# Optimization experiments

Hardware: AMD Instinct MI355X
Metric: run time of the kernel (lower is better)

The kernel has to match this reference:

```python
import jax, jax.numpy as jnp
import numpy as np

SEQ, BS, IN, H, NUM_LAYERS = 512, 64, 1024, 1024, 2


def setup_inputs() -> dict:
    key = jax.random.key(0)
    k1, k2, k3, k4 = jax.random.split(key, 4)

    def xavier(k, shape):
        fan_in, fan_out = shape
        lim = jnp.sqrt(6.0 / (fan_in + fan_out))
        return jax.random.uniform(k, shape, jnp.float32, -lim, lim)

    return {
        "x": jax.random.normal(k1, (SEQ, BS, IN), jnp.float32),
        "W_ii0": xavier(k2, (IN, 4 * H)),
        "W_ii": xavier(k3, (H, 4 * H)),
        "W_hi": xavier(k4, (H, 4 * H)),
        "bias": jnp.zeros((4 * H,), jnp.float32),
    }


def _run_layer(x, W_in, W_hi, bias, hidden):
    # x: [seq, bs, feat]; precompute input projection for all timesteps at once
    xw = jnp.einsum('sbf,fg->sbg', x, W_in) + bias  # [seq, bs, 4H]
    bs = x.shape[1]

    def step(carry, xw_t):
        h, c = carry
        gates = xw_t + h @ W_hi  # [bs, 4H]
        i_t = jax.nn.sigmoid(gates[:, :hidden])
        f_t = jax.nn.sigmoid(gates[:, hidden:2 * hidden])
        g_t = jnp.tanh(gates[:, 2 * hidden:3 * hidden])
        o_t = jax.nn.sigmoid(gates[:, 3 * hidden:])
        c = f_t * c + i_t * g_t
        h = o_t * jnp.tanh(c)
        return (h, c), h

    h0 = jnp.zeros((bs, hidden), x.dtype)
    c0 = jnp.zeros((bs, hidden), x.dtype)
    (h, c), hs = jax.lax.scan(step, (h0, c0), xw)
    return hs, h, c  # hs: [seq, bs, hidden]


def reference(x, W_ii0, W_ii, W_hi, bias):
    h = c = None
    for l in range(NUM_LAYERS):
        W_in = W_ii0 if l == 0 else W_ii
        x, h, c = _run_layer(x, W_in, W_hi, bias, H)
    return x, (h, c)
```

## Files before the change

kernel.cpp:

```cpp
#include <hip/hip_runtime.h>

typedef __attribute__((ext_vector_type(8))) short short8;
typedef __attribute__((ext_vector_type(4))) short short4v;
typedef __attribute__((ext_vector_type(4))) float floatx4;

#define SEQ 512
#define BS  64
#define HID 1024
#define G4  4096
#define NBLK 128
#define NGRP 4
#define BPG  32
#define GBS  16
#define UPB  32

__device__ __forceinline__ unsigned short f2b(float f) {
  union { float f; unsigned u; } v; v.f = f;
  return (unsigned short)((v.u + 0x7FFFu + ((v.u >> 16) & 1u)) >> 16);
}
__device__ __forceinline__ float b2f(unsigned short s) {
  union { unsigned u; float f; } v; v.u = ((unsigned)s) << 16;
  return v.f;
}

__device__ __forceinline__ void gload_lds16_cc(const void* g, void* l) {
  __builtin_amdgcn_global_load_lds(
      (const __attribute__((address_space(1))) unsigned int*)g,
      (__attribute__((address_space(3))) unsigned int*)l,
      16, 0, 17);
}

__global__ void wtrans(const float* __restrict__ W, short* __restrict__ WT) {
  __shared__ float tile[32][33];
  const int tx = threadIdx.x, ty = threadIdx.y;
  const int n0 = blockIdx.x << 5, k0 = blockIdx.y << 5;
#pragma unroll
  for (int i = 0; i < 32; i += 8)
    tile[ty + i][tx] = W[(size_t)(k0 + ty + i) * G4 + n0 + tx];
  __syncthreads();
#pragma unroll
  for (int i = 0; i < 32; i += 8)
    WT[(size_t)(n0 + ty + i) * 1024 + k0 + tx] = (short)f2b(tile[tx][ty + i]);
}

__global__ __launch_bounds__(256)
void conv_bf16(const float* __restrict__ in, unsigned short* __restrict__ out) {
  const size_t i = ((size_t)blockIdx.x * 256 + threadIdx.x) * 8;
  const floatx4 a = *(const floatx4*)(in + i);
  const floatx4 b = *(const floatx4*)(in + i + 4);
  short8 s;
#pragma unroll
  for (int e = 0; e < 4; ++e) { s[e] = (short)f2b(a[e]); s[4 + e] = (short)f2b(b[e]); }
  *(short8*)(out + i) = s;
}

struct FusedArgs {
  const unsigned short* xw;
  const short* wt_hi;
  unsigned short* hbuf;
  float* cbuf;
  unsigned int* flags;
  float* hs;
  unsigned short* hsb;
  float* h_final;
  float* c_final;
  int t0, t1, wr_final;
  const short* A;
  const short* BT;
  const float* bias;
  unsigned short* dst;
  int Mrows, genable;
};

__device__ __forceinline__ void scan_body(const FusedArgs& p, char* smem) {
  float* gsm = (float*)(smem + 32768);
  const int tid = threadIdx.x;
  const int wave = tid >> 6, lane = tid & 63;
  const int lr = lane & 15, lh = lane >> 4;
  const int nt = wave >> 1;
  const int kh = wave & 1;
  const int blk = blockIdx.x;
  const int g = blk >> 5;
  const int ub_idx = blk & 31;
  const int gcol = ((nt >> 1) << 10) + ub_idx * UPB + ((nt & 1) << 4) + lr;

  short8 breg[16];
  {
    const short* wp = p.wt_hi + (size_t)gcol * HID + (kh << 9) + (lh << 3);
#pragma unroll
    for (int kk = 0; kk < 16; ++kk) breg[kk] = *(const short8*)(wp + (kk << 5));
  }

  const int b_loc = tid >> 5, u_loc = tid & 31;
  const int ci = ((g * GBS + b_loc) << 10) + ub_idx * UPB + u_loc;
  float creg = (tid < 512) ? p.cbuf[ci] : 0.f;

  const int asw = lr & 7;
  const unsigned long long fad =
      (unsigned long long)(p.flags + ((size_t)(g * BPG) + (lane & 31)) * 16);

  for (int t = p.t0; t < p.t1; ++t) {
    float xv[4] = {0.f, 0.f, 0.f, 0.f};
    if (kh == 0) {
#pragma unroll
      for (int r = 0; r < 4; ++r) {
        const size_t rowi = (size_t)(t - p.t0) * BS + g * GBS + (lh << 2) + r;
        xv[r] = b2f(p.xw[rowi * G4 + gcol]);
      }
    }

    if (t > 0 && wave == 0) {
      unsigned f0;
      for (;;) {
        asm volatile("global_load_dword %0, %1, off sc0 sc1\n\t"
                     "s_waitcnt vmcnt(0)"
                     : "=v"(f0) : "v"(fad) : "memory");
        if (__all(f0 >= (unsigned)t)) break;
        __builtin_amdgcn_s_sleep(1);
      }
    }
    __syncthreads();

    const unsigned short* hb = p.hbuf + (size_t)(t & 1) * (BS * HID) + (size_t)g * GBS * HID;
    unsigned short* hw = p.hbuf + (size_t)((t + 1) & 1) * (BS * HID) + (size_t)g * GBS * HID;

#pragma unroll
    for (int j = 0; j < 2; ++j) {
      const int i = (wave << 1) + j;
      const int row = i >> 1, half = i & 1;
      const int chunk = ((half << 6) + lane) ^ (row & 7);
      gload_lds16_cc(hb + row * HID + (chunk << 3), smem + (i << 10));
    }
    asm volatile("s_waitcnt vmcnt(0)" ::: "memory");
    __builtin_amdgcn_s_barrier();

    floatx4 acc = {0.f, 0.f, 0.f, 0.f};
#pragma unroll
    for (int kk = 0; kk < 16; ++kk) {
      const int kc = (kh << 6) + (kk << 2) + lh;
      const short8 afr = *(const short8*)(smem + (lr << 11) + ((kc ^ asw) << 4));
      acc = __builtin_amdgcn_mfma_f32_16x16x32_bf16(afr, breg[kk], acc, 0, 0, 0);
    }

    {
      const int gate = nt >> 1, ub16 = (nt & 1) << 4;
#pragma unroll
      for (int r = 0; r < 4; ++r) {
        const int b = (lh << 2) + r;
        gsm[((kh << 2) + gate) * 528 + b * 33 + ub16 + lr] = acc[r] + xv[r];
      }
    }
    __syncthreads();

    float hv = 0.f, cn = 0.f;
    unsigned hv16 = 0;
    if (tid < 512) {
      const int o = b_loc * 33 + u_loc;
      const float ig = gsm[o]            + gsm[4 * 528 + o];
      const float fg = gsm[1 * 528 + o]  + gsm[5 * 528 + o];
      const float gg = gsm[2 * 528 + o]  + gsm[6 * 528 + o];
      const float og = gsm[3 * 528 + o]  + gsm[7 * 528 + o];
      const float iv = 1.f / (1.f + __expf(-ig));
      const float fv = 1.f / (1.f + __expf(-fg));
      const float gv = tanhf(gg);
      const float ov = 1.f / (1.f + __expf(-og));
      cn = fv * creg + iv * gv;
      creg = cn;
      hv = ov * tanhf(cn);
      hv16 = (unsigned)f2b(hv);
      const unsigned other = (unsigned)__shfl_xor((int)hv16, 1, 64);
      if ((u_loc & 1) == 0) {
        const unsigned val = (hv16 & 0xFFFFu) | (other << 16);
        const unsigned long long dst =
            (unsigned long long)(hw + (size_t)b_loc * HID + ub_idx * UPB + u_loc);
        asm volatile("global_store_dword %0, %1, off sc0 sc1"
                     :: "v"(dst), "v"(val) : "memory");
      }
    }
    asm volatile("s_waitcnt vmcnt(0)" ::: "memory");
    __syncthreads();
    if (tid == 0) {
      const unsigned long long fdst = (unsigned long long)(p.flags + (size_t)blk * 16);
      const unsigned fval = (unsigned)(t + 1);
      asm volatile("global_store_dword %0, %1, off sc0 sc1"
                   :: "v"(fdst), "v"(fval) : "memory");
    }
    if (tid < 512) {
      const size_t oidx = ((size_t)t * BS + g * GBS + b_loc) * HID + ub_idx * UPB + u_loc;
      p.hs[oidx] = hv;
      p.hsb[oidx] = (unsigned short)hv16;
      if (p.wr_final && t == SEQ - 1) { p.h_final[ci] = hv; p.c_final[ci] = cn; }
    }
  }
  if (tid < 512) p.cbuf[ci] = creg;
}

__device__ __forceinline__ void gemm_body(const FusedArgs& p, char* smem, int bi) {
  if (!p.genable) return;
  short* Al = (short*)smem;
  short* Bl = (short*)(smem + 10240);
  const int tid = threadIdx.x;
  const int wave = tid >> 6, lane = tid & 63;
  const int lr = lane & 15, lh = lane >> 4;
  const int wm = wave >> 2, wn = wave & 3;
  const int nmt = p.Mrows >> 7;
  const int tot = nmt << 5;
  const int srow = tid >> 3, scol = (tid & 7) << 2;

  for (int tt = bi; tt < tot; tt += NBLK) {
    const int m0 = (tt >> 5) << 7, n0 = (tt & 31) << 7;
    const short* aptr = p.A + (size_t)(m0 + srow) * 1024 + scol;
    const short* bptr = p.BT + (size_t)(n0 + srow) * 1024 + scol;
    floatx4 acc[2][2] = {};
    short4v pa = *(const short4v*)aptr;
    short4v pb = *(const short4v*)bptr;
    for (int it = 0; it < 32; ++it) {
      __syncthreads();
      *(short4v*)&Al[srow * 40 + scol] = pa;
      *(short4v*)&Bl[srow * 40 + scol] = pb;
      __syncthreads();
      if (it < 31) {
        pa = *(const short4v*)(aptr + ((it + 1) << 5));
        pb = *(const short4v*)(bptr + ((it + 1) << 5));
      }
      short8 af[2], bf[2];
#pragma unroll
      for (int mt = 0; mt < 2; ++mt)
        af[mt] = *(const short8*)&Al[(wm * 32 + mt * 16 + lr) * 40 + lh * 8];
#pragma unroll
      for (int nt = 0; nt < 2; ++nt)
        bf[nt] = *(const short8*)&Bl[(wn * 32 + nt * 16 + lr) * 40 + lh * 8];
#pragma unroll
      for (int mt = 0; mt < 2; ++mt)
#pragma unroll
        for (int nt = 0; nt < 2; ++nt)
          acc[mt][nt] = __builtin_amdgcn_mfma_f32_16x16x32_bf16(af[mt], bf[nt], acc[mt][nt], 0, 0, 0);
    }
#pragma unroll
    for (int nt = 0; nt < 2; ++nt) {
      const int gc = n0 + wn * 32 + nt * 16 + lr;
      const float bv = p.bias[gc];
#pragma unroll
      for (int mt = 0; mt < 2; ++mt)
#pragma unroll
        for (int r = 0; r < 4; ++r) {
          const int gr = m0 + wm * 32 + mt * 16 + (lh << 2) + r;
          p.dst[(size_t)gr * G4 + gc] = f2b(acc[mt][nt][r] + bv);
        }
    }
  }
}

__global__ __launch_bounds__(1024)
void gemm_pre(FusedArgs p) {
  __shared__ __align__(16) char smem[84480];
  gemm_body(p, smem, blockIdx.x);
}

__global__ __launch_bounds__(1024)
void lstm_fused(FusedArgs p) {
  __shared__ __align__(16) char smem[84480];
  if (blockIdx.x < NBLK) scan_body(p, smem);
  else                   gemm_body(p, smem, blockIdx.x - NBLK);
}

extern "C" void kernel_launch(void* const* d_in, const int* in_sizes, int n_in,
                              void* d_out, int out_size, void* d_ws, size_t ws_size,
                              hipStream_t stream) {
  const float* x    = (const float*)d_in[0];
  const float* Wii0 = (const float*)d_in[1];
  const float* Wii  = (const float*)d_in[2];
  const float* Whi  = (const float*)d_in[3];
  const float* bias = (const float*)d_in[4];
  float* out  = (float*)d_out;
  float* hs   = out;
  float* hfin = out + (size_t)SEQ * BS * HID;
  float* cfin = hfin + BS * HID;

  char* ws = (char*)d_ws;
  short* WT0 = (short*)ws;
  short* WT1 = WT0 + (size_t)G4 * 1024;
  short* WTh = WT1 + (size_t)G4 * 1024;
  unsigned short* hbuf = (unsigned short*)(WTh + (size_t)G4 * 1024);
  float* cbuf = (float*)(hbuf + 2 * BS * HID);
  unsigned int* flags = (unsigned int*)(cbuf + BS * HID);
  unsigned short* xb = (unsigned short*)(flags + NBLK * 16);
  char* tail = (char*)(xb + (size_t)SEQ * BS * HID);
  const size_t head = (size_t)(tail - ws);
  const size_t avail = (ws_size > head) ? ws_size - head : 0;
  const size_t perT = (size_t)BS * G4 * 2;

  int chunk;
  if      (avail >= 2 * 128 * perT) chunk = 128;
  else if (avail >= 2 * 64  * perT) chunk = 64;
  else if (avail >= 2 * 32  * perT) chunk = 32;
  else                              chunk = 8;
  const size_t chunkBytes = (size_t)chunk * perT;
  unsigned short* xwbuf[2] = { (unsigned short*)tail,
                               (unsigned short*)(tail + chunkBytes) };
  const int nc = SEQ / chunk;

  wtrans<<<dim3(128, 32), dim3(32, 8), 0, stream>>>(Wii0, WT0);
  wtrans<<<dim3(128, 32), dim3(32, 8), 0, stream>>>(Wii, WT1);
  wtrans<<<dim3(128, 32), dim3(32, 8), 0, stream>>>(Whi, WTh);
  conv_bf16<<<dim3((SEQ * BS * HID) / (256 * 8)), dim3(256), 0, stream>>>(x, xb);

  for (int layer = 0; layer < 2; ++layer) {
    hipMemsetAsync(hbuf, 0, 2 * BS * HID * sizeof(unsigned short), stream);
    hipMemsetAsync(cbuf, 0, BS * HID * sizeof(float), stream);
    hipMemsetAsync(flags, 0, NBLK * 16 * sizeof(unsigned int), stream);

    if (layer == 0) {
      FusedArgs pa = {};
      pa.A = (const short*)xb;
      pa.BT = WT0;
      pa.bias = bias;
      pa.dst = xwbuf[0];
      pa.Mrows = chunk * BS;
      pa.genable = 1;
      gemm_pre<<<dim3(NBLK), dim3(1024), 0, stream>>>(pa);
    }

    for (int c = 0; c < nc; ++c) {
      FusedArgs fa;
      fa.xw = xwbuf[c & 1];
      fa.wt_hi = WTh;
      fa.hbuf = hbuf;
      fa.cbuf = cbuf;
      fa.flags = flags;
      fa.hs = hs;
      fa.hsb = xb;
      fa.h_final = layer ? hfin : nullptr;
      fa.c_final = layer ? cfin : nullptr;
      fa.t0 = c * chunk;
      fa.t1 = (c + 1) * chunk;
      fa.wr_final = layer;
      fa.bias = bias;
      fa.dst = xwbuf[(c + 1) & 1];
      fa.Mrows = chunk * BS;
      const int nxt = ((c + 1) % nc) * chunk * BS;
      fa.A = (const short*)(xb + (size_t)nxt * HID);
      fa.BT = (layer == 0 && c < nc - 1) ? WT0 : WT1;
      fa.genable = !(layer == 1 && c == nc - 1);
      void* args[] = { &fa };
      hipLaunchCooperativeKernel(reinterpret_cast<const void*>(&lstm_fused),
                                 dim3(2 * NBLK), dim3(1024), args, 0u, stream);
    }
  }
}
```

Measured before the change: 3.941 ms.

## Halve block size; load recurrent h directly into registers, drop K-split

Cuts both the scan and GEMM blocks from 1024 to 512 threads. In the scan, each wave now covers the full K dimension with 32 weight fragments held in registers. The hidden-state A-fragments are loaded straight from global memory into registers with double-buffered, coherent dwordx4 loads, replacing the LDS staging, its barrier and the two-way K-split reduction. The GEMM side gives each wave a wider 32x64 tile using 16-byte staging loads to match the smaller block. This shortens the per-timestep critical path, at the cost of much higher register pressure and more redundant global reads of h across waves.

```diff
diff --git a/kernel.cpp b/kernel.cpp
--- a/kernel.cpp
+++ b/kernel.cpp
@@ -1,7 +1,6 @@
 #include <hip/hip_runtime.h>
 
 typedef __attribute__((ext_vector_type(8))) short short8;
-typedef __attribute__((ext_vector_type(4))) short short4v;
 typedef __attribute__((ext_vector_type(4))) float floatx4;
 
 #define SEQ 512
@@ -21,13 +20,6 @@
 __device__ __forceinline__ float b2f(unsigned short s) {
   union { unsigned u; float f; } v; v.u = ((unsigned)s) << 16;
   return v.f;
-}
-
-__device__ __forceinline__ void gload_lds16_cc(const void* g, void* l) {
-  __builtin_amdgcn_global_load_lds(
-      (const __attribute__((address_space(1))) unsigned int*)g,
-      (__attribute__((address_space(3))) unsigned int*)l,
-      16, 0, 17);
 }
 
 __global__ void wtrans(const float* __restrict__ W, short* __restrict__ WT) {
@@ -73,40 +65,36 @@
 };
 
 __device__ __forceinline__ void scan_body(const FusedArgs& p, char* smem) {
-  float* gsm = (float*)(smem + 32768);
+  float* gsm = (float*)smem;
   const int tid = threadIdx.x;
   const int wave = tid >> 6, lane = tid & 63;
   const int lr = lane & 15, lh = lane >> 4;
-  const int nt = wave >> 1;
-  const int kh = wave & 1;
+  const int gate = wave >> 1, uh = wave & 1;
   const int blk = blockIdx.x;
   const int g = blk >> 5;
   const int ub_idx = blk & 31;
-  const int gcol = ((nt >> 1) << 10) + ub_idx * UPB + ((nt & 1) << 4) + lr;
-
-  short8 breg[16];
+  const int gcol = (gate << 10) + ub_idx * UPB + (uh << 4) + lr;
+
+  short8 breg[32];
   {
-    const short* wp = p.wt_hi + (size_t)gcol * HID + (kh << 9) + (lh << 3);
-#pragma unroll
-    for (int kk = 0; kk < 16; ++kk) breg[kk] = *(const short8*)(wp + (kk << 5));
+    const short* wp = p.wt_hi + (size_t)gcol * HID + (lh << 3);
+#pragma unroll
+    for (int kk = 0; kk < 32; ++kk) breg[kk] = *(const short8*)(wp + (kk << 5));
   }
 
   const int b_loc = tid >> 5, u_loc = tid & 31;
   const int ci = ((g * GBS + b_loc) << 10) + ub_idx * UPB + u_loc;
-  float creg = (tid < 512) ? p.cbuf[ci] : 0.f;
-
-  const int asw = lr & 7;
+  float creg = p.cbuf[ci];
+
   const unsigned long long fad =
       (unsigned long long)(p.flags + ((size_t)(g * BPG) + (lane & 31)) * 16);
 
   for (int t = p.t0; t < p.t1; ++t) {
-    float xv[4] = {0.f, 0.f, 0.f, 0.f};
-    if (kh == 0) {
-#pragma unroll
-      for (int r = 0; r < 4; ++r) {
-        const size_t rowi = (size_t)(t - p.t0) * BS + g * GBS + (lh << 2) + r;
-        xv[r] = b2f(p.xw[rowi * G4 + gcol]);
-      }
+    float xv[4];
+#pragma unroll
+    for (int r = 0; r < 4; ++r) {
+      const size_t rowi = (size_t)(t - p.t0) * BS + g * GBS + (lh << 2) + r;
+      xv[r] = b2f(p.xw[rowi * G4 + gcol]);
     }
 
     if (t > 0 && wave == 0) {
@@ -121,53 +109,60 @@
     }
     __syncthreads();
 
-    const unsigned short* hb = p.hbuf + (size_t)(t & 1) * (BS * HID) + (size_t)g * GBS * HID;
+    const unsigned long long ab = (unsigned long long)((const char*)p.hbuf
+        + (size_t)(t & 1) * (BS * HID * 2) + (size_t)g * GBS * 2048
+        + (size_t)lr * 2048 + (lh << 4));
+
+    short8 aA[8], aB[8];
+#pragma unroll
+    for (int j = 0; j < 8; ++j)
+      asm volatile("global_load_dwordx4 %0, %1, off offset:%c2 sc0 sc1"
+                   : "=v"(aA[j]) : "v"(ab), "i"(j << 6) : "memory");
+    floatx4 acc = {0.f, 0.f, 0.f, 0.f};
+#pragma unroll
+    for (int gg = 0; gg < 4; ++gg) {
+      if (gg < 3) {
+#pragma unroll
+        for (int j = 0; j < 8; ++j) {
+          short8& dstv = (gg & 1) ? aA[j] : aB[j];
+          asm volatile("global_load_dwordx4 %0, %1, off offset:%c2 sc0 sc1"
+                       : "=v"(dstv) : "v"(ab), "i"(((gg + 1) << 9) + (j << 6))
+                       : "memory");
+        }
+        asm volatile("s_waitcnt vmcnt(8)" ::: "memory");
+      } else {
+        asm volatile("s_waitcnt vmcnt(0)" ::: "memory");
+      }
+      __builtin_amdgcn_sched_barrier(0);
+#pragma unroll
+      for (int j = 0; j < 8; ++j) {
+        const short8 af = (gg & 1) ? aB[j] : aA[j];
+        acc = __builtin_amdgcn_mfma_f32_16x16x32_bf16(af, breg[(gg << 3) + j], acc, 0, 0, 0);
+      }
+    }
+
+#pragma unroll
+    for (int r = 0; r < 4; ++r) {
+      const int b = (lh << 2) + r;
+      gsm[((gate << 4) + b) * 33 + (uh << 4) + lr] = acc[r] + xv[r];
+    }
+    __syncthreads();
+
+    const int o = (b_loc) * 33 + u_loc;
+    const float ig = gsm[o];
+    const float fg = gsm[(16 << 0) * 33 + o];
+    const float gg2 = gsm[(32) * 33 + o];
+    const float og = gsm[(48) * 33 + o];
+    const float iv = 1.f / (1.f + __expf(-ig));
+    const float fv = 1.f / (1.f + __expf(-fg));
+    const float gv = tanhf(gg2);
+    const float ov = 1.f / (1.f + __expf(-og));
+    const float cn = fv * creg + iv * gv;
+    creg = cn;
+    const float hv = ov * tanhf(cn);
+    const unsigned hv16 = (unsigned)f2b(hv);
     unsigned short* hw = p.hbuf + (size_t)((t + 1) & 1) * (BS * HID) + (size_t)g * GBS * HID;
-
-#pragma unroll
-    for (int j = 0; j < 2; ++j) {
-      const int i = (wave << 1) + j;
-      const int row = i >> 1, half = i & 1;
-      const int chunk = ((half << 6) + lane) ^ (row & 7);
-      gload_lds16_cc(hb + row * HID + (chunk << 3), smem + (i << 10));
-    }
-    asm volatile("s_waitcnt vmcnt(0)" ::: "memory");
-    __builtin_amdgcn_s_barrier();
-
-    floatx4 acc = {0.f, 0.f, 0.f, 0.f};
-#pragma unroll
-    for (int kk = 0; kk < 16; ++kk) {
-      const int kc = (kh << 6) + (kk << 2) + lh;
-      const short8 afr = *(const short8*)(smem + (lr << 11) + ((kc ^ asw) << 4));
-      acc = __builtin_amdgcn_mfma_f32_16x16x32_bf16(afr, breg[kk], acc, 0, 0, 0);
-    }
-
     {
-      const int gate = nt >> 1, ub16 = (nt & 1) << 4;
-#pragma unroll
-      for (int r = 0; r < 4; ++r) {
-        const int b = (lh << 2) + r;
-        gsm[((kh << 2) + gate) * 528 + b * 33 + ub16 + lr] = acc[r] + xv[r];
-      }
-    }
-    __syncthreads();
-
-    float hv = 0.f, cn = 0.f;
-    unsigned hv16 = 0;
-    if (tid < 512) {
-      const int o = b_loc * 33 + u_loc;
-      const float ig = gsm[o]            + gsm[4 * 528 + o];
-      const float fg = gsm[1 * 528 + o]  + gsm[5 * 528 + o];
-      const float gg = gsm[2 * 528 + o]  + gsm[6 * 528 + o];
-      const float og = gsm[3 * 528 + o]  + gsm[7 * 528 + o];
-      const float iv = 1.f / (1.f + __expf(-ig));
-      const float fv = 1.f / (1.f + __expf(-fg));
-      const float gv = tanhf(gg);
-      const float ov = 1.f / (1.f + __expf(-og));
-      cn = fv * creg + iv * gv;
-      creg = cn;
-      hv = ov * tanhf(cn);
-      hv16 = (unsigned)f2b(hv);
       const unsigned other = (unsigned)__shfl_xor((int)hv16, 1, 64);
       if ((u_loc & 1) == 0) {
         const unsigned val = (hv16 & 0xFFFFu) | (other << 16);
@@ -185,14 +180,14 @@
       asm volatile("global_store_dword %0, %1, off sc0 sc1"
                    :: "v"(fdst), "v"(fval) : "memory");
     }
-    if (tid < 512) {
+    {
       const size_t oidx = ((size_t)t * BS + g * GBS + b_loc) * HID + ub_idx * UPB + u_loc;
       p.hs[oidx] = hv;
       p.hsb[oidx] = (unsigned short)hv16;
       if (p.wr_final && t == SEQ - 1) { p.h_final[ci] = hv; p.c_final[ci] = cn; }
     }
   }
-  if (tid < 512) p.cbuf[ci] = creg;
+  p.cbuf[ci] = creg;
 }
 
 __device__ __forceinline__ void gemm_body(const FusedArgs& p, char* smem, int bi) {
@@ -202,43 +197,43 @@
   const int tid = threadIdx.x;
   const int wave = tid >> 6, lane = tid & 63;
   const int lr = lane & 15, lh = lane >> 4;
-  const int wm = wave >> 2, wn = wave & 3;
+  const int wm = wave >> 1, wn = wave & 1;
   const int nmt = p.Mrows >> 7;
   const int tot = nmt << 5;
-  const int srow = tid >> 3, scol = (tid & 7) << 2;
+  const int srow = tid >> 2, scol = (tid & 3) << 3;
 
   for (int tt = bi; tt < tot; tt += NBLK) {
     const int m0 = (tt >> 5) << 7, n0 = (tt & 31) << 7;
     const short* aptr = p.A + (size_t)(m0 + srow) * 1024 + scol;
     const short* bptr = p.BT + (size_t)(n0 + srow) * 1024 + scol;
-    floatx4 acc[2][2] = {};
-    short4v pa = *(const short4v*)aptr;
-    short4v pb = *(const short4v*)bptr;
+    floatx4 acc[2][4] = {};
+    short8 pa = *(const short8*)aptr;
+    short8 pb = *(const short8*)bptr;
     for (int it = 0; it < 32; ++it) {
       __syncthreads();
-      *(short4v*)&Al[srow * 40 + scol] = pa;
-      *(short4v*)&Bl[srow * 40 + scol] = pb;
+      *(short8*)&Al[srow * 40 + scol] = pa;
+      *(short8*)&Bl[srow * 40 + scol] = pb;
       __syncthreads();
       if (it < 31) {
-        pa = *(const short4v*)(aptr + ((it + 1) << 5));
-        pb = *(const short4v*)(bptr + ((it + 1) << 5));
-      }
-      short8 af[2], bf[2];
+        pa = *(const short8*)(aptr + ((it + 1) << 5));
+        pb = *(const short8*)(bptr + ((it + 1) << 5));
+      }
+      short8 af[2], bf[4];
 #pragma unroll
       for (int mt = 0; mt < 2; ++mt)
         af[mt] = *(const short8*)&Al[(wm * 32 + mt * 16 + lr) * 40 + lh * 8];
 #pragma unroll
-      for (int nt = 0; nt < 2; ++nt)
-        bf[nt] = *(const short8*)&Bl[(wn * 32 + nt * 16 + lr) * 40 + lh * 8];
+      for (int nt = 0; nt < 4; ++nt)
+        bf[nt] = *(const short8*)&Bl[(wn * 64 + nt * 16 + lr) * 40 + lh * 8];
 #pragma unroll
       for (int mt = 0; mt < 2; ++mt)
 #pragma unroll
-        for (int nt = 0; nt < 2; ++nt)
+        for (int nt = 0; nt < 4; ++nt)
           acc[mt][nt] = __builtin_amdgcn_mfma_f32_16x16x32_bf16(af[mt], bf[nt], acc[mt][nt], 0, 0, 0);
     }
 #pragma unroll
-    for (int nt = 0; nt < 2; ++nt) {
-      const int gc = n0 + wn * 32 + nt * 16 + lr;
+    for (int nt = 0; nt < 4; ++nt) {
+      const int gc = n0 + wn * 64 + nt * 16 + lr;
       const float bv = p.bias[gc];
 #pragma unroll
       for (int mt = 0; mt < 2; ++mt)
@@ -251,13 +246,13 @@
   }
 }
 
-__global__ __launch_bounds__(1024)
+__global__ __launch_bounds__(512, 2)
 void gemm_pre(FusedArgs p) {
   __shared__ __align__(16) char smem[84480];
   gemm_body(p, smem, blockIdx.x);
 }
 
-__global__ __launch_bounds__(1024)
+__global__ __launch_bounds__(512, 2)
 void lstm_fused(FusedArgs p) {
   __shared__ __align__(16) char smem[84480];
   if (blockIdx.x < NBLK) scan_body(p, smem);
@@ -318,7 +313,7 @@
       pa.dst = xwbuf[0];
       pa.Mrows = chunk * BS;
       pa.genable = 1;
-      gemm_pre<<<dim3(NBLK), dim3(1024), 0, stream>>>(pa);
+      gemm_pre<<<dim3(NBLK), dim3(512), 0, stream>>>(pa);
     }
 
     for (int c = 0; c < nc; ++c) {
@@ -344,7 +339,7 @@
       fa.genable = !(layer == 1 && c == nc - 1);
       void* args[] = { &fa };
       hipLaunchCooperativeKernel(reinterpret_cast<const void*>(&lstm_fused),
-                                 dim3(2 * NBLK), dim3(1024), args, 0u, stream);
+                                 dim3(2 * NBLK), dim3(512), args, 0u, stream);
     }
   }
 }
```

Measured after the change: 9.900 ms. 2.51x slower.
